# Kernel tuning notes

Measured on AMD Instinct MI355X. Metric: run time of the kernel, lower is better.

## Reference

```python
import jax, jax.numpy as jnp
import numpy as np

DEPTH, DIM, DH, H, DQ, V = 4, 1024, 4096, 8, 128, 32000
B, L = 2, 1024


def setup_inputs() -> dict:
    key = jax.random.key(0)
    ks = iter(jax.random.split(key, 48))
    def nrm(shape, scale=1.0):
        return jax.random.normal(next(ks), shape, jnp.float32) * scale
    d = {}
    d["x"] = nrm((B, L, V))
    d["tin_w"] = nrm((DIM, V), V ** -0.5)
    d["tin_b"] = nrm((DIM,), 0.02)
    d["tout_w"] = nrm((V, DIM), DIM ** -0.5)
    d["tout_b"] = nrm((V,), 0.02)
    d["wq_w"] = nrm((DEPTH, H * DQ, DIM), DIM ** -0.5)
    d["wq_b"] = nrm((DEPTH, H * DQ), 0.02)
    d["wk_w"] = nrm((DEPTH, H * DQ, DIM), DIM ** -0.5)
    d["wk_b"] = nrm((DEPTH, H * DQ), 0.02)
    d["wv_w"] = nrm((DEPTH, H * DQ, DIM), DIM ** -0.5)
    d["wv_b"] = nrm((DEPTH, H * DQ), 0.02)
    d["wo_w"] = nrm((DEPTH, DIM, H * DQ), (H * DQ) ** -0.5)
    d["wo_b"] = nrm((DEPTH, DIM), 0.02)
    d["f1_w"] = nrm((DEPTH, DH, DIM), DIM ** -0.5)
    d["f1_b"] = nrm((DEPTH, DH), 0.02)
    d["f2_w"] = nrm((DEPTH, DIM, DH), DH ** -0.5)
    d["f2_b"] = nrm((DEPTH, DIM), 0.02)
    d["phz_re"] = nrm((DEPTH, H, DQ))
    d["phz_im"] = nrm((DEPTH, H, DQ))
    d["amp"] = nrm((DEPTH, H))
    d["lc_re"] = nrm((DEPTH, H, DQ, DQ), 0.02)
    d["lc_im"] = nrm((DEPTH, H, DQ, DQ), 0.02)
    return d


def _layernorm(x):
    m = x.mean(-1, keepdims=True)
    v = ((x - m) ** 2).mean(-1, keepdims=True)
    return (x - m) * jax.lax.rsqrt(v + 1e-5)


def _retention(x, qw, qb, kw, kb, vw, vb, ow, ob, pre, pim, amp, lcr, lci):
    b, l, _ = x.shape
    q = (x @ qw.T + qb).reshape(b, l, H, DQ)
    k = (x @ kw.T + kb).reshape(b, l, H, DQ)
    v = (x @ vw.T + vb).reshape(b, l, H, DQ)
    pz = pre + 1j * pim                              # [H,DQ] complex
    phase = pz / jnp.abs(pz)                         # unit modulus
    a = jax.nn.sigmoid(amp)                          # [H]
    phazor = phase * a[:, None]
    n = jnp.arange(l)
    pp = phase[None, :, :] ** n[:, None, None]       # [L,H,DQ]
    pp_inv = phase[None, :, :] ** (-n)[:, None, None]
    php = phazor[None, :, :] ** n[:, None, None]
    lc = jax.lax.stop_gradient(lcr + 1j * lci)       # [H,DQ,DQ], detached in torch
    qc = q.astype(jnp.complex64)
    kc = k.astype(jnp.complex64)
    vc = v.astype(jnp.complex64)
    cross = jnp.einsum('blhd,lhd,hde->blhe', qc, php * phazor[None], lc)
    tril = n[:, None] >= n[None, :]
    expn = jnp.where(tril, n[:, None] - n[None, :], 0)           # [L,L]
    mask = jnp.where(tril[None], a[:, None, None] ** expn[None], 0.0)  # [H,L,L]
    qk = jnp.einsum('blhd,bmhd->bhlm', qc * pp[None], kc * pp_inv[None])
    inner = jnp.einsum('bhlm,bmhd->blhd', qk * mask[None].astype(jnp.complex64), vc)
    y = jax.nn.silu((inner + cross).real).reshape(b, l, H * DQ)
    return y @ ow.T + ob


def reference(x, tin_w, tin_b, tout_w, tout_b, wq_w, wq_b, wk_w, wk_b, wv_w, wv_b,
              wo_w, wo_b, f1_w, f1_b, f2_w, f2_b, phz_re, phz_im, amp, lc_re, lc_im):
    h = x @ tin_w.T + tin_b
    for i in range(DEPTH):
        r = _retention(_layernorm(h), wq_w[i], wq_b[i], wk_w[i], wk_b[i],
                       wv_w[i], wv_b[i], wo_w[i], wo_b[i],
                       phz_re[i], phz_im[i], amp[i], lc_re[i], lc_im[i])
        h = h + r
        f = _layernorm(h)
        f = jax.nn.silu(f @ f1_w[i].T + f1_b[i]) @ f2_w[i].T + f2_b[i]
        h = h + f
    return h @ tout_w.T + tout_b
```

## Files before the change

kernel.cpp:

```cpp
#include <hip/hip_runtime.h>
#include <hip/hip_bf16.h>
#include <stdint.h>

#define DEPTH 4
#define DIM   1024
#define DH    4096
#define NH    8
#define DQ    128
#define VOC   32000
#define BATCH 2
#define SEQ   1024
#define ROWS  (BATCH*SEQ)

#define PQKV  ((long long)ROWS*DIM)
#define PQKV3 ((long long)ROWS*3*DIM)
#define PROT  ((long long)BATCH*NH*SEQ*2*DQ)
#define PVT   ((long long)BATCH*NH*DQ*SEQ)
#define PS    ((long long)BATCH*NH*SEQ*SEQ)
#define PMID  ((long long)ROWS*DH)
#define PY    ((long long)ROWS*DIM)

typedef __hip_bfloat16 bf16;
using f32x4  = __attribute__((ext_vector_type(4))) float;
using bf16x8 = __attribute__((ext_vector_type(8))) __bf16;

__device__ __forceinline__ unsigned short bcu(bf16 h) {
  return __builtin_bit_cast(unsigned short, h);
}

__device__ __forceinline__ void wpair(bf16* p, long long off, long long plane, float v) {
  bf16 hi = __float2bfloat16(v);
  p[off] = hi;
  p[off + plane] = __float2bfloat16(v - __bfloat162float(hi));
}

__device__ __forceinline__ void gload_lds16(const void* g, void* l) {
  __builtin_amdgcn_global_load_lds(
      (const __attribute__((address_space(1))) void*)g,
      (__attribute__((address_space(3))) void*)(uintptr_t)l,
      16, 0, 0);
}

#define BM 128
#define BN 128
#define BKK 64
#define PL 16384

template<int EPI, int SA, int SB>
__global__ __launch_bounds__(256, (SA || SB) ? 2 : 4)
void gemm_bt(const bf16* __restrict__ A, long long sA, long long pA, int lda,
             const bf16* __restrict__ B, long long sB, long long pB, int ldb, int bmod,
             void* __restrict__ Cv, long long sC, long long pC, int ldc,
             const float* __restrict__ bias, int hmod,
             int M, int N, int K, int ksplit, int causal)
{
  __shared__ int4 sbuf[1024 * (2 + SA + SB)];
  char* Asb = (char*)sbuf;
  char* Bsb = Asb + PL * (1 + SA);

  const int tid  = threadIdx.x;
  const int lane = tid & 63;
  const int wave = tid >> 6;
  const int wr   = wave >> 1;
  const int wc   = wave & 1;
  const int z    = blockIdx.z;
  const int zb   = z / ksplit;
  const int ks   = z - zb * ksplit;
  const int Kc   = K / ksplit;
  const int k0   = ks * Kc;
  const int tm   = blockIdx.x * BM;
  const int tn   = blockIdx.y * BN;

  if (causal == 1 && tn >= tm + BM) return;
  int kend = k0 + Kc;
  if (causal == 2) {
    kend = min(kend, tm + BM);
    if (kend <= k0) return;
  }

  const bf16* Ab = A + (long long)zb * sA;
  const bf16* Bb = B + (long long)(zb % bmod) * sB;

  f32x4 acc[4][4] = {};

  for (int kt = k0; kt < kend; kt += BKK) {
#pragma unroll
    for (int j = 0; j < 4; ++j) {
      int slot0 = j*256 + wave*64;
      int i = slot0 + lane;
      int row = i >> 3;
      int gc  = (i & 7) ^ (row & 7);
      long long ga = (long long)(tm + row) * lda + kt + gc*8;
      long long gb = (long long)(tn + row) * ldb + kt + gc*8;
      gload_lds16(Ab + ga, Asb + slot0*16);
      if (SA) gload_lds16(Ab + pA + ga, Asb + PL + slot0*16);
      gload_lds16(Bb + gb, Bsb + slot0*16);
      if (SB) gload_lds16(Bb + pB + gb, Bsb + PL + slot0*16);
    }
    __syncthreads();
#pragma unroll
    for (int kh = 0; kh < 2; ++kh) {
      const int cb = kh*4 + (lane >> 4);
      int4 avh[4], bvh[4], avl[4], bvl[4];
#pragma unroll
      for (int mi = 0; mi < 4; ++mi) {
        int m = wr*64 + mi*16 + (lane & 15);
        int off = m*128 + ((cb ^ (m & 7)) << 4);
        avh[mi] = *(const int4*)(Asb + off);
        if (SA) avl[mi] = *(const int4*)(Asb + PL + off);
      }
#pragma unroll
      for (int nj = 0; nj < 4; ++nj) {
        int n = wc*64 + nj*16 + (lane & 15);
        int off = n*128 + ((cb ^ (n & 7)) << 4);
        bvh[nj] = *(const int4*)(Bsb + off);
        if (SB) bvl[nj] = *(const int4*)(Bsb + PL + off);
      }
#pragma unroll
      for (int mi = 0; mi < 4; ++mi)
#pragma unroll
        for (int nj = 0; nj < 4; ++nj)
          acc[mi][nj] = __builtin_amdgcn_mfma_f32_16x16x32_bf16(
              __builtin_bit_cast(bf16x8, avh[mi]),
              __builtin_bit_cast(bf16x8, bvh[nj]), acc[mi][nj], 0, 0, 0);
      if (SA)
#pragma unroll
        for (int mi = 0; mi < 4; ++mi)
#pragma unroll
          for (int nj = 0; nj < 4; ++nj)
            acc[mi][nj] = __builtin_amdgcn_mfma_f32_16x16x32_bf16(
                __builtin_bit_cast(bf16x8, avl[mi]),
                __builtin_bit_cast(bf16x8, bvh[nj]), acc[mi][nj], 0, 0, 0);
      if (SB)
#pragma unroll
        for (int mi = 0; mi < 4; ++mi)
#pragma unroll
          for (int nj = 0; nj < 4; ++nj)
            acc[mi][nj] = __builtin_amdgcn_mfma_f32_16x16x32_bf16(
                __builtin_bit_cast(bf16x8, avh[mi]),
                __builtin_bit_cast(bf16x8, bvl[nj]), acc[mi][nj], 0, 0, 0);
    }
    __syncthreads();
  }

  const float* dtab = (EPI == 7) ? bias + (zb % hmod) * (SEQ + 1) : nullptr;
  const int col = lane & 15;
  const int rb  = (lane >> 4) << 2;
  float* Cf = (float*)Cv + (long long)zb * sC;
  bf16*  Ch = (bf16*) Cv + (long long)zb * sC;

#pragma unroll
  for (int mi = 0; mi < 4; ++mi)
#pragma unroll
    for (int nj = 0; nj < 4; ++nj) {
      long long gn = tn + wc*64 + nj*16 + col;
      float bv_ = (EPI != 7 && bias && ks == 0) ? bias[gn] : 0.f;
#pragma unroll
      for (int r = 0; r < 4; ++r) {
        long long gm = tm + wr*64 + mi*16 + rb + r;
        float v = acc[mi][nj][r] + bv_;
        long long off = gm * (long long)ldc + gn;
        if (EPI == 0)      Cf[off] = v;
        else if (EPI == 3) { if (ksplit > 1) atomicAdd(&Cf[off], v); else Cf[off] += v; }
        else if (EPI == 5) wpair(Ch, off, pC, v);
        else if (EPI == 6) wpair(Ch, off, pC, v / (1.f + __expf(-v)));
        else {
          long long dlt = gm - gn;
          float dcy = (dlt >= 0) ? dtab[dlt] : 0.f;
          Ch[off] = __float2bfloat16(acc[mi][nj][r] * dcy);
        }
      }
    }
}

__global__ void castw_kernel(const float* __restrict__ wq, const float* __restrict__ wk,
                             const float* __restrict__ wv, const float* __restrict__ wo,
                             const float* __restrict__ f1, const float* __restrict__ f2,
                             bf16* __restrict__ Wqkv, bf16* __restrict__ Wol,
                             bf16* __restrict__ Wf1, bf16* __restrict__ Wf2) {
  const long long S1 = (long long)DIM*DIM;
  const long long S4 = S1 >> 2;
  const long long WP = 3*S1;
  long long i = (long long)blockIdx.x * blockDim.x + threadIdx.x;
  const float* src; bf16 *hi, *lo; long long j4;
  if (i < 3*S4) {
    int t = (int)(i / S4);
    src = (t == 0) ? wq : (t == 1) ? wk : wv;
    j4 = i - (long long)t * S4;
    hi = Wqkv + (long long)t * S1; lo = hi + WP;
  } else if (i < 4*S4)  { src = wo; j4 = i - 3*S4; hi = Wol; lo = Wol + S1; }
  else if (i < 8*S4)    { src = f1; j4 = i - 4*S4; hi = Wf1; lo = Wf1 + 4*S1; }
  else if (i < 12*S4)   { src = f2; j4 = i - 8*S4; hi = Wf2; lo = nullptr; }
  else return;
  float4 v = ((const float4*)src)[j4];
  bf16 h0 = __float2bfloat16(v.x), h1 = __float2bfloat16(v.y);
  bf16 h2 = __float2bfloat16(v.z), h3 = __float2bfloat16(v.w);
  ((ushort4*)hi)[j4] = ushort4{bcu(h0), bcu(h1), bcu(h2), bcu(h3)};
  if (lo) {
    bf16 l0 = __float2bfloat16(v.x - __bfloat162float(h0));
    bf16 l1 = __float2bfloat16(v.y - __bfloat162float(h1));
    bf16 l2 = __float2bfloat16(v.z - __bfloat162float(h2));
    bf16 l3 = __float2bfloat16(v.w - __bfloat162float(h3));
    ((ushort4*)lo)[j4] = ushort4{bcu(l0), bcu(l1), bcu(l2), bcu(l3)};
  }
}

#define MISC_LC   (NH*DQ*DQ)
#define MISC_B3   (MISC_LC + 3*DIM)
#define MISC_DC   (MISC_B3 + NH*(SEQ+1))
#define MISC_ZR   (MISC_DC + (BATCH*NH*SEQ*DQ)/4)
__global__ void misc_kernel(const float* __restrict__ lcr, const float* __restrict__ lci,
                            bf16* __restrict__ lc,
                            const float* __restrict__ bq, const float* __restrict__ bk,
                            const float* __restrict__ bv, float* __restrict__ qkvbi,
                            const float* __restrict__ amp, float* __restrict__ dtab,
                            float4* __restrict__ retz) {
  long long i = (long long)blockIdx.x * blockDim.x + threadIdx.x;
  if (i < MISC_LC) {
    int d = i & 127, e = (i >> 7) & 127, h = i >> 14;
    float vr = lcr[((long long)h*DQ + d)*DQ + e];
    float vi = lci[((long long)h*DQ + d)*DQ + e];
    long long dst = ((long long)h*DQ + e)*(2*DQ) + d;
    lc[dst]      = __float2bfloat16(vr);
    lc[dst + DQ] = __float2bfloat16(-vi);
  } else if (i < MISC_B3) {
    int j = (int)(i - MISC_LC);
    qkvbi[j] = (j < DIM) ? bq[j] : (j < 2*DIM) ? bk[j - DIM] : bv[j - 2*DIM];
  } else if (i < MISC_DC) {
    int j = (int)(i - MISC_B3);
    int h = j / (SEQ+1), n = j % (SEQ+1);
    float a = 1.f / (1.f + __expf(-amp[h]));
    dtab[j] = powf(a, (float)n);
  } else if (i < MISC_ZR) {
    retz[i - MISC_DC] = float4{0.f, 0.f, 0.f, 0.f};
  }
}

#define TIN_X4 ((long long)ROWS*VOC/4)
#define TIN_W4 (TIN_X4 + (long long)DIM*VOC/4)
#define TIN_H4 (TIN_W4 + (long long)ROWS*DIM/4)
__global__ void tinprep_kernel(const float* __restrict__ x, bf16* __restrict__ xb,
                               const float* __restrict__ tw, bf16* __restrict__ twb,
                               float4* __restrict__ hz) {
  long long i = (long long)blockIdx.x * blockDim.x + threadIdx.x;
  const float* src; bf16* dst; long long j;
  if (i < TIN_X4)      { src = x;  dst = xb;  j = i; }
  else if (i < TIN_W4) { src = tw; dst = twb; j = i - TIN_X4; }
  else if (i < TIN_H4) { hz[i - TIN_W4] = float4{0.f,0.f,0.f,0.f}; return; }
  else return;
  float4 v = ((const float4*)src)[j];
  ushort4 o{bcu(__float2bfloat16(v.x)), bcu(__float2bfloat16(v.y)),
            bcu(__float2bfloat16(v.z)), bcu(__float2bfloat16(v.w))};
  ((ushort4*)dst)[j] = o;
}

#define TAIL_H (PQKV)
#define TAIL_W (TAIL_H + (long long)VOC*DIM/4)
__global__ void tailprep_kernel(const float* __restrict__ h, bf16* __restrict__ hb,
                                const float* __restrict__ tw, bf16* __restrict__ twb) {
  long long i = (long long)blockIdx.x * blockDim.x + threadIdx.x;
  if (i < TAIL_H) {
    float v = h[i];
    bf16 hi = __float2bfloat16(v);
    hb[i] = hi;
    hb[i + PQKV] = __float2bfloat16(v - __bfloat162float(hi));
  } else if (i < TAIL_W) {
    long long j = i - TAIL_H;
    float4 v = ((const float4*)tw)[j];
    ushort4 o{bcu(__float2bfloat16(v.x)), bcu(__float2bfloat16(v.y)),
              bcu(__float2bfloat16(v.z)), bcu(__float2bfloat16(v.w))};
    ((ushort4*)twb)[j] = o;
  }
}

__global__ void ln_kernel(const float* __restrict__ in, bf16* __restrict__ out) {
  const int row = blockIdx.x;
  const int tid = threadIdx.x;
  const float4 v = ((const float4*)(in + (size_t)row*DIM))[tid];
  float s  = v.x + v.y + v.z + v.w;
  float s2 = v.x*v.x + v.y*v.y + v.z*v.z + v.w*v.w;
#pragma unroll
  for (int o = 32; o > 0; o >>= 1) { s += __shfl_xor(s, o); s2 += __shfl_xor(s2, o); }
  __shared__ float red[8];
  const int wv = tid >> 6;
  if ((tid & 63) == 0) { red[wv] = s; red[4 + wv] = s2; }
  __syncthreads();
  s  = red[0] + red[1] + red[2] + red[3];
  s2 = red[4] + red[5] + red[6] + red[7];
  const float mean = s * (1.f / DIM);
  const float var  = s2 * (1.f / DIM) - mean * mean;
  const float inv  = rsqrtf(var + 1e-5f);
  long long base = (long long)row*DIM + tid*4;
  wpair(out, base + 0, PQKV, (v.x - mean) * inv);
  wpair(out, base + 1, PQKV, (v.y - mean) * inv);
  wpair(out, base + 2, PQKV, (v.z - mean) * inv);
  wpair(out, base + 3, PQKV, (v.w - mean) * inv);
}

__global__ void rotate_kernel(const bf16* __restrict__ qkv,
                              const float* __restrict__ pre, const float* __restrict__ pim,
                              const float* __restrict__ dtab,
                              bf16* __restrict__ qrot, bf16* __restrict__ krot,
                              bf16* __restrict__ qwb) {
  const int d = threadIdx.x, l = blockIdx.x, h = blockIdx.y, b = blockIdx.z;
  const float tr = pre[h*DQ + d], ti = pim[h*DQ + d];
  const float theta = atan2f(ti, tr);
  const long long rowb = (long long)(b*SEQ + l)*(3*DIM) + h*DQ + d;
  const float qv = __bfloat162float(qkv[rowb]) + __bfloat162float(qkv[rowb + PQKV3]);
  const float kv = __bfloat162float(qkv[rowb + DIM]) + __bfloat162float(qkv[rowb + DIM + PQKV3]);
  float sn, cs;
  sincosf(theta * (float)l, &sn, &cs);
  const long long dst = ((long long)(b*NH + h)*SEQ + l)*(2*DQ) + d;
  qrot[dst]      = __float2bfloat16(qv * cs);
  qrot[dst + DQ] = __float2bfloat16(qv * sn);
  krot[dst]      = __float2bfloat16(kv * cs);
  krot[dst + DQ] = __float2bfloat16(kv * sn);
  float sn2, cs2;
  sincosf(theta * (float)(l + 1), &sn2, &cs2);
  const float ad = dtab[h*(SEQ+1) + l + 1];
  qwb[dst]      = __float2bfloat16(qv * ad * cs2);
  qwb[dst + DQ] = __float2bfloat16(qv * ad * sn2);
}

__global__ void vt_kernel(const bf16* __restrict__ qkv, bf16* __restrict__ vt) {
  __shared__ float tile[64][65];
  const int t  = threadIdx.x;
  const int c  = t & 63, r4 = t >> 6;
  const int m0 = blockIdx.x * 64;
  const int d0 = blockIdx.y * 64;
  const int h  = blockIdx.z & (NH - 1);
  const int b  = blockIdx.z >> 3;
#pragma unroll
  for (int rr = 0; rr < 64; rr += 4) {
    const int m = m0 + rr + r4;
    const long long src = (long long)(b*SEQ + m)*(3*DIM) + 2*DIM + h*DQ + d0 + c;
    tile[rr + r4][c] = __bfloat162float(qkv[src]) + __bfloat162float(qkv[src + PQKV3]);
  }
  __syncthreads();
#pragma unroll
  for (int rr = 0; rr < 64; rr += 4) {
    const int d = rr + r4;
    vt[((long long)(b*NH + h)*DQ + d0 + d)*SEQ + m0 + c] = __float2bfloat16(tile[c][d]);
  }
}

__global__ void siluret_kernel(const float* __restrict__ ret, bf16* __restrict__ y) {
  const int d = threadIdx.x, l = blockIdx.x, h = blockIdx.y, b = blockIdx.z;
  float r = ret[((long long)(b*NH + h)*SEQ + l)*DQ + d];
  float s = r / (1.f + __expf(-r));
  wpair(y, ((long long)(b*SEQ + l)*NH + h)*DQ + d, PY, s);
}

extern "C" void kernel_launch(void* const* d_in, const int* in_sizes, int n_in,
                              void* d_out, int out_size, void* d_ws, size_t ws_size,
                              hipStream_t stream) {
  const float* x      = (const float*)d_in[0];
  const float* tin_w  = (const float*)d_in[1];
  const float* tin_b  = (const float*)d_in[2];
  const float* tout_w = (const float*)d_in[3];
  const float* tout_b = (const float*)d_in[4];
  const float* wq_w   = (const float*)d_in[5];
  const float* wq_b   = (const float*)d_in[6];
  const float* wk_w   = (const float*)d_in[7];
  const float* wk_b   = (const float*)d_in[8];
  const float* wv_w   = (const float*)d_in[9];
  const float* wv_b   = (const float*)d_in[10];
  const float* wo_w   = (const float*)d_in[11];
  const float* wo_b   = (const float*)d_in[12];
  const float* f1_w   = (const float*)d_in[13];
  const float* f1_b   = (const float*)d_in[14];
  const float* f2_w   = (const float*)d_in[15];
  const float* f2_b   = (const float*)d_in[16];
  const float* phz_re = (const float*)d_in[17];
  const float* phz_im = (const float*)d_in[18];
  const float* amp    = (const float*)d_in[19];
  const float* lc_re  = (const float*)d_in[20];
  const float* lc_im  = (const float*)d_in[21];
  (void)in_sizes; (void)n_in; (void)out_size; (void)ws_size;

  char* w = (char*)d_ws;
  auto alloc = [&](size_t bytes) {
    char* p = w; w += (bytes + 255) & ~(size_t)255; return p;
  };
  auto palloc = [&](long long elems) {
    return (bf16*)alloc((size_t)elems * 2 * 2);
  };

  const long long WP = 3LL*DIM*DIM;
  float* h     = (float*)alloc((size_t)ROWS*DIM*4);
  float* ret   = (float*)alloc((size_t)BATCH*NH*SEQ*DQ*4);
  float* qkvbi = (float*)alloc((size_t)3*DIM*4);
  float* dtab  = (float*)alloc((size_t)NH*(SEQ+1)*4);
  bf16*  hb    = palloc(PQKV);
  bf16*  Wqkv  = palloc(WP);
  bf16*  Wol   = palloc((long long)DIM*DIM);
  bf16*  Wf1l  = palloc((long long)DH*DIM);
  bf16*  Wf2l  = (bf16*)alloc((size_t)DIM*DH*2);
  bf16*  qkvb  = palloc(PQKV3);
  bf16*  lcc   = (bf16*)alloc((size_t)NH*DQ*2*DQ*2);
  bf16*  Wbig  = (bf16*)alloc((size_t)DIM*VOC*2);
  bf16*  qrot  = (bf16*)alloc((size_t)PROT*2);
  bf16*  krot  = (bf16*)alloc((size_t)PROT*2);
  bf16*  qwb   = (bf16*)alloc((size_t)PROT*2);
  bf16*  vtb   = (bf16*)alloc((size_t)PVT*2);
  bf16*  Sb    = (bf16*)alloc((size_t)PS*2);
  bf16*  mid   = palloc(PMID);
  bf16*  xb = (bf16*)d_out;
  bf16*  yb = qkvb;

  auto gemm = [&](int epi, int sa, int sb, const bf16* A, long long sA, long long pA, int lda,
                  const bf16* B, long long sB, long long pB, int ldb, int bmod,
                  void* C, long long sC, long long pC, int ldc,
                  const float* bias, int hmod, int M, int N, int K, int batch,
                  int ksplit, int causal) {
    dim3 g(M / BM, N / BN, batch * ksplit), blk(256);
    if (epi == 3 && !sa && !sb)      gemm_bt<3,0,0><<<g, blk, 0, stream>>>(A,sA,pA,lda,B,sB,pB,ldb,bmod,C,sC,pC,ldc,bias,hmod,M,N,K,ksplit,causal);
    else if (epi == 7)               gemm_bt<7,0,0><<<g, blk, 0, stream>>>(A,sA,pA,lda,B,sB,pB,ldb,bmod,C,sC,pC,ldc,bias,hmod,M,N,K,ksplit,causal);
    else if (epi == 0 && sa && !sb)  gemm_bt<0,1,0><<<g, blk, 0, stream>>>(A,sA,pA,lda,B,sB,pB,ldb,bmod,C,sC,pC,ldc,bias,hmod,M,N,K,ksplit,causal);
    else if (epi == 3 && sa && !sb)  gemm_bt<3,1,0><<<g, blk, 0, stream>>>(A,sA,pA,lda,B,sB,pB,ldb,bmod,C,sC,pC,ldc,bias,hmod,M,N,K,ksplit,causal);
    else if (epi == 3)               gemm_bt<3,1,1><<<g, blk, 0, stream>>>(A,sA,pA,lda,B,sB,pB,ldb,bmod,C,sC,pC,ldc,bias,hmod,M,N,K,ksplit,causal);
    else if (epi == 5)               gemm_bt<5,1,1><<<g, blk, 0, stream>>>(A,sA,pA,lda,B,sB,pB,ldb,bmod,C,sC,pC,ldc,bias,hmod,M,N,K,ksplit,causal);
    else if (epi == 6)               gemm_bt<6,1,1><<<g, blk, 0, stream>>>(A,sA,pA,lda,B,sB,pB,ldb,bmod,C,sC,pC,ldc,bias,hmod,M,N,K,ksplit,causal);
  };
  const int BIG = 1 << 30;

  tinprep_kernel<<<dim3((unsigned)((TIN_H4 + 255) / 256)), dim3(256), 0, stream>>>(
      x, xb, tin_w, Wbig, (float4*)h);
  gemm(3, 0, 0, xb, 0, 0, VOC, Wbig, 0, 0, VOC, BIG, h, 0, 0, DIM, tin_b, 1,
       ROWS, DIM, VOC, 1, 10, 0);

  for (int i = 0; i < DEPTH; ++i) {
    {
      long long tot4 = 12LL * ((long long)DIM*DIM >> 2);
      castw_kernel<<<dim3((unsigned)((tot4 + 255) / 256)), dim3(256), 0, stream>>>(
          wq_w + (size_t)i*DIM*DIM, wk_w + (size_t)i*DIM*DIM, wv_w + (size_t)i*DIM*DIM,
          wo_w + (size_t)i*DIM*DIM, f1_w + (size_t)i*DH*DIM, f2_w + (size_t)i*DIM*DH,
          Wqkv, Wol, Wf1l, Wf2l);
      misc_kernel<<<dim3((unsigned)((MISC_ZR + 255) / 256)), dim3(256), 0, stream>>>(
          lc_re + (size_t)i*NH*DQ*DQ, lc_im + (size_t)i*NH*DQ*DQ, lcc,
          wq_b + i*DIM, wk_b + i*DIM, wv_b + i*DIM, qkvbi,
          amp + i*NH, dtab, (float4*)ret);
    }

    ln_kernel<<<ROWS, 256, 0, stream>>>(h, hb);
    gemm(5, 1, 1, hb, 0, PQKV, DIM, Wqkv, 0, WP, DIM, BIG,
         qkvb, 0, PQKV3, 3*DIM, qkvbi, 1, ROWS, 3*DIM, DIM, 1, 1, 0);
    rotate_kernel<<<dim3(SEQ, NH, BATCH), DQ, 0, stream>>>(
        qkvb, phz_re + i*NH*DQ, phz_im + i*NH*DQ, dtab, qrot, krot, qwb);
    vt_kernel<<<dim3(SEQ/64, DQ/64, BATCH*NH), 256, 0, stream>>>(qkvb, vtb);
    gemm(7, 0, 0, qrot, (long long)SEQ*2*DQ, 0, 2*DQ,
         krot, (long long)SEQ*2*DQ, 0, 2*DQ, BIG,
         Sb, (long long)SEQ*SEQ, 0, SEQ, dtab, NH, SEQ, SEQ, 2*DQ, BATCH*NH, 1, 1);
    gemm(3, 0, 0, Sb, (long long)SEQ*SEQ, 0, SEQ,
         vtb, (long long)DQ*SEQ, 0, SEQ, BIG,
         ret, (long long)SEQ*DQ, 0, DQ, nullptr, 1, SEQ, DQ, SEQ, BATCH*NH, 4, 2);
    gemm(3, 0, 0, qwb, (long long)SEQ*2*DQ, 0, 2*DQ,
         lcc, (long long)DQ*2*DQ, 0, 2*DQ, NH,
         ret, (long long)SEQ*DQ, 0, DQ, nullptr, 1, SEQ, DQ, 2*DQ, BATCH*NH, 2, 0);
    siluret_kernel<<<dim3(SEQ, NH, BATCH), DQ, 0, stream>>>(ret, yb);
    gemm(3, 1, 1, yb, 0, PY, DIM, Wol, 0, (long long)DIM*DIM, DIM, BIG,
         h, 0, 0, DIM, wo_b + i*DIM, 1, ROWS, DIM, DIM, 1, 2, 0);

    ln_kernel<<<ROWS, 256, 0, stream>>>(h, hb);
    gemm(6, 1, 1, hb, 0, PQKV, DIM, Wf1l, 0, (long long)DH*DIM, DIM, BIG,
         mid, 0, PMID, DH, f1_b + i*DH, 1, ROWS, DH, DIM, 1, 1, 0);
    gemm(3, 1, 0, mid, 0, PMID, DH, Wf2l, 0, 0, DH, BIG,
         h, 0, 0, DIM, f2_b + i*DIM, 1, ROWS, DIM, DH, 1, 4, 0);
  }

  tailprep_kernel<<<dim3((unsigned)((TAIL_W + 255) / 256)), dim3(256), 0, stream>>>(
      h, hb, tout_w, Wbig);
  gemm(0, 1, 0, hb, 0, PQKV, DIM, Wbig, 0, 0, DIM, BIG,
       (float*)d_out, 0, 0, VOC, tout_b, 1, ROWS, VOC, DIM, 1, 1, 0);
}
```

Measured before the change: 1.814 ms.

## Fuse cross-term GEMM into retention S·V GEMM via concatenated K dimension

The cross term (qw @ lc) is folded into the S·V GEMM by widening its K dimension: the qw block is stored in the first 256 columns of an extended score buffer and lc in the first 256 columns of an extended V-transpose buffer, so one GEMM computes both. This removes one GEMM launch and one atomic-accumulate pass over the output. The weight-cast and misc prep kernels are merged into a single launch, atan2 for the phases is precomputed once per layer, and the layernorm stores are vectorized. The causal K bound is shifted to include the prefix columns, at the cost of larger buffers and a more complex indexing scheme.

Result: faster. 1.739 ms, median of 2 (-4.1%).

```diff
diff --git a/kernel.cpp b/kernel.cpp
--- a/kernel.cpp
+++ b/kernel.cpp
@@ -11,12 +11,12 @@
 #define BATCH 2
 #define SEQ   1024
 #define ROWS  (BATCH*SEQ)
+#define CROSSK 256
+#define LDS_X (CROSSK + SEQ)
 
 #define PQKV  ((long long)ROWS*DIM)
 #define PQKV3 ((long long)ROWS*3*DIM)
 #define PROT  ((long long)BATCH*NH*SEQ*2*DQ)
-#define PVT   ((long long)BATCH*NH*DQ*SEQ)
-#define PS    ((long long)BATCH*NH*SEQ*SEQ)
 #define PMID  ((long long)ROWS*DH)
 #define PY    ((long long)ROWS*DIM)
 
@@ -74,7 +74,7 @@
   if (causal == 1 && tn >= tm + BM) return;
   int kend = k0 + Kc;
   if (causal == 2) {
-    kend = min(kend, tm + BM);
+    kend = min(kend, tm + BM + CROSSK);
     if (kend <= k0) return;
   }
 
@@ -173,66 +173,77 @@
     }
 }
 
-__global__ void castw_kernel(const float* __restrict__ wq, const float* __restrict__ wk,
-                             const float* __restrict__ wv, const float* __restrict__ wo,
-                             const float* __restrict__ f1, const float* __restrict__ f2,
-                             bf16* __restrict__ Wqkv, bf16* __restrict__ Wol,
-                             bf16* __restrict__ Wf1, bf16* __restrict__ Wf2) {
-  const long long S1 = (long long)DIM*DIM;
-  const long long S4 = S1 >> 2;
-  const long long WP = 3*S1;
-  long long i = (long long)blockIdx.x * blockDim.x + threadIdx.x;
-  const float* src; bf16 *hi, *lo; long long j4;
-  if (i < 3*S4) {
-    int t = (int)(i / S4);
-    src = (t == 0) ? wq : (t == 1) ? wk : wv;
-    j4 = i - (long long)t * S4;
-    hi = Wqkv + (long long)t * S1; lo = hi + WP;
-  } else if (i < 4*S4)  { src = wo; j4 = i - 3*S4; hi = Wol; lo = Wol + S1; }
-  else if (i < 8*S4)    { src = f1; j4 = i - 4*S4; hi = Wf1; lo = Wf1 + 4*S1; }
-  else if (i < 12*S4)   { src = f2; j4 = i - 8*S4; hi = Wf2; lo = nullptr; }
-  else return;
-  float4 v = ((const float4*)src)[j4];
-  bf16 h0 = __float2bfloat16(v.x), h1 = __float2bfloat16(v.y);
-  bf16 h2 = __float2bfloat16(v.z), h3 = __float2bfloat16(v.w);
-  ((ushort4*)hi)[j4] = ushort4{bcu(h0), bcu(h1), bcu(h2), bcu(h3)};
-  if (lo) {
-    bf16 l0 = __float2bfloat16(v.x - __bfloat162float(h0));
-    bf16 l1 = __float2bfloat16(v.y - __bfloat162float(h1));
-    bf16 l2 = __float2bfloat16(v.z - __bfloat162float(h2));
-    bf16 l3 = __float2bfloat16(v.w - __bfloat162float(h3));
-    ((ushort4*)lo)[j4] = ushort4{bcu(l0), bcu(l1), bcu(l2), bcu(l3)};
-  }
-}
-
-#define MISC_LC   (NH*DQ*DQ)
-#define MISC_B3   (MISC_LC + 3*DIM)
-#define MISC_DC   (MISC_B3 + NH*(SEQ+1))
-#define MISC_ZR   (MISC_DC + (BATCH*NH*SEQ*DQ)/4)
-__global__ void misc_kernel(const float* __restrict__ lcr, const float* __restrict__ lci,
-                            bf16* __restrict__ lc,
+#define MC_LC (NH*DQ*DQ)
+#define MC_TH (MC_LC + NH*DQ)
+#define MC_B3 (MC_TH + 3*DIM)
+#define MC_DC (MC_B3 + NH*(SEQ+1))
+#define MC_ZR (MC_DC + (BATCH*NH*SEQ*DQ)/4)
+__global__ void prep_kernel(const float* __restrict__ wq, const float* __restrict__ wk,
+                            const float* __restrict__ wv, const float* __restrict__ wo,
+                            const float* __restrict__ f1, const float* __restrict__ f2,
+                            bf16* __restrict__ Wqkv, bf16* __restrict__ Wol,
+                            bf16* __restrict__ Wf1, bf16* __restrict__ Wf2,
+                            const float* __restrict__ lcr, const float* __restrict__ lci,
+                            bf16* __restrict__ vte,
+                            const float* __restrict__ pre, const float* __restrict__ pim,
+                            float* __restrict__ theta,
                             const float* __restrict__ bq, const float* __restrict__ bk,
                             const float* __restrict__ bv, float* __restrict__ qkvbi,
                             const float* __restrict__ amp, float* __restrict__ dtab,
                             float4* __restrict__ retz) {
+  const long long S1 = (long long)DIM*DIM;
+  const long long S4 = S1 >> 2;
+  const long long WPq = 3*S1;
+  const long long CW4 = 12*S4;
   long long i = (long long)blockIdx.x * blockDim.x + threadIdx.x;
-  if (i < MISC_LC) {
-    int d = i & 127, e = (i >> 7) & 127, h = i >> 14;
+  if (i < CW4) {
+    const float* src; bf16 *hi, *lo; long long j4;
+    if (i < 3*S4) {
+      int t = (int)(i / S4);
+      src = (t == 0) ? wq : (t == 1) ? wk : wv;
+      j4 = i - (long long)t * S4;
+      hi = Wqkv + (long long)t * S1; lo = hi + WPq;
+    } else if (i < 4*S4)  { src = wo; j4 = i - 3*S4; hi = Wol; lo = Wol + S1; }
+    else if (i < 8*S4)    { src = f1; j4 = i - 4*S4; hi = Wf1; lo = Wf1 + 4*S1; }
+    else                  { src = f2; j4 = i - 8*S4; hi = Wf2; lo = nullptr; }
+    float4 v = ((const float4*)src)[j4];
+    bf16 h0 = __float2bfloat16(v.x), h1 = __float2bfloat16(v.y);
+    bf16 h2 = __float2bfloat16(v.z), h3 = __float2bfloat16(v.w);
+    ((ushort4*)hi)[j4] = ushort4{bcu(h0), bcu(h1), bcu(h2), bcu(h3)};
+    if (lo) {
+      bf16 l0 = __float2bfloat16(v.x - __bfloat162float(h0));
+      bf16 l1 = __float2bfloat16(v.y - __bfloat162float(h1));
+      bf16 l2 = __float2bfloat16(v.z - __bfloat162float(h2));
+      bf16 l3 = __float2bfloat16(v.w - __bfloat162float(h3));
+      ((ushort4*)lo)[j4] = ushort4{bcu(l0), bcu(l1), bcu(l2), bcu(l3)};
+    }
+    return;
+  }
+  long long j = i - CW4;
+  if (j < MC_LC) {
+    int d = (int)(j & 127), e = (int)((j >> 7) & 127), h = (int)(j >> 14);
     float vr = lcr[((long long)h*DQ + d)*DQ + e];
     float vi = lci[((long long)h*DQ + d)*DQ + e];
-    long long dst = ((long long)h*DQ + e)*(2*DQ) + d;
-    lc[dst]      = __float2bfloat16(vr);
-    lc[dst + DQ] = __float2bfloat16(-vi);
-  } else if (i < MISC_B3) {
-    int j = (int)(i - MISC_LC);
-    qkvbi[j] = (j < DIM) ? bq[j] : (j < 2*DIM) ? bk[j - DIM] : bv[j - 2*DIM];
-  } else if (i < MISC_DC) {
-    int j = (int)(i - MISC_B3);
-    int h = j / (SEQ+1), n = j % (SEQ+1);
+    bf16 br = __float2bfloat16(vr), bi = __float2bfloat16(-vi);
+#pragma unroll
+    for (int b = 0; b < BATCH; ++b) {
+      long long base = ((long long)(b*NH + h)*DQ + e) * LDS_X;
+      vte[base + d]      = br;
+      vte[base + DQ + d] = bi;
+    }
+  } else if (j < MC_TH) {
+    int t = (int)(j - MC_LC);
+    theta[t] = atan2f(pim[t], pre[t]);
+  } else if (j < MC_B3) {
+    int t = (int)(j - MC_TH);
+    qkvbi[t] = (t < DIM) ? bq[t] : (t < 2*DIM) ? bk[t - DIM] : bv[t - 2*DIM];
+  } else if (j < MC_DC) {
+    int t = (int)(j - MC_B3);
+    int h = t / (SEQ+1), n = t % (SEQ+1);
     float a = 1.f / (1.f + __expf(-amp[h]));
-    dtab[j] = powf(a, (float)n);
-  } else if (i < MISC_ZR) {
-    retz[i - MISC_DC] = float4{0.f, 0.f, 0.f, 0.f};
+    dtab[t] = powf(a, (float)n);
+  } else if (j < MC_ZR) {
+    retz[j - MC_DC] = float4{0.f, 0.f, 0.f, 0.f};
   }
 }
 
@@ -290,21 +301,25 @@
   const float mean = s * (1.f / DIM);
   const float var  = s2 * (1.f / DIM) - mean * mean;
   const float inv  = rsqrtf(var + 1e-5f);
-  long long base = (long long)row*DIM + tid*4;
-  wpair(out, base + 0, PQKV, (v.x - mean) * inv);
-  wpair(out, base + 1, PQKV, (v.y - mean) * inv);
-  wpair(out, base + 2, PQKV, (v.z - mean) * inv);
-  wpair(out, base + 3, PQKV, (v.w - mean) * inv);
+  float e0 = (v.x - mean) * inv, e1 = (v.y - mean) * inv;
+  float e2 = (v.z - mean) * inv, e3 = (v.w - mean) * inv;
+  bf16 h0 = __float2bfloat16(e0), h1 = __float2bfloat16(e1);
+  bf16 h2 = __float2bfloat16(e2), h3 = __float2bfloat16(e3);
+  bf16 l0 = __float2bfloat16(e0 - __bfloat162float(h0));
+  bf16 l1 = __float2bfloat16(e1 - __bfloat162float(h1));
+  bf16 l2 = __float2bfloat16(e2 - __bfloat162float(h2));
+  bf16 l3 = __float2bfloat16(e3 - __bfloat162float(h3));
+  ((ushort4*)(out + (size_t)row*DIM))[tid]        = ushort4{bcu(h0), bcu(h1), bcu(h2), bcu(h3)};
+  ((ushort4*)(out + PQKV + (size_t)row*DIM))[tid] = ushort4{bcu(l0), bcu(l1), bcu(l2), bcu(l3)};
 }
 
 __global__ void rotate_kernel(const bf16* __restrict__ qkv,
-                              const float* __restrict__ pre, const float* __restrict__ pim,
+                              const float* __restrict__ theta_t,
                               const float* __restrict__ dtab,
                               bf16* __restrict__ qrot, bf16* __restrict__ krot,
-                              bf16* __restrict__ qwb) {
+                              bf16* __restrict__ SbX) {
   const int d = threadIdx.x, l = blockIdx.x, h = blockIdx.y, b = blockIdx.z;
-  const float tr = pre[h*DQ + d], ti = pim[h*DQ + d];
-  const float theta = atan2f(ti, tr);
+  const float theta = theta_t[h*DQ + d];
   const long long rowb = (long long)(b*SEQ + l)*(3*DIM) + h*DQ + d;
   const float qv = __bfloat162float(qkv[rowb]) + __bfloat162float(qkv[rowb + PQKV3]);
   const float kv = __bfloat162float(qkv[rowb + DIM]) + __bfloat162float(qkv[rowb + DIM + PQKV3]);
@@ -318,11 +333,12 @@
   float sn2, cs2;
   sincosf(theta * (float)(l + 1), &sn2, &cs2);
   const float ad = dtab[h*(SEQ+1) + l + 1];
-  qwb[dst]      = __float2bfloat16(qv * ad * cs2);
-  qwb[dst + DQ] = __float2bfloat16(qv * ad * sn2);
-}
-
-__global__ void vt_kernel(const bf16* __restrict__ qkv, bf16* __restrict__ vt) {
+  const long long qw = ((long long)(b*NH + h)*SEQ + l)*LDS_X + d;
+  SbX[qw]      = __float2bfloat16(qv * ad * cs2);
+  SbX[qw + DQ] = __float2bfloat16(qv * ad * sn2);
+}
+
+__global__ void vt_kernel(const bf16* __restrict__ qkv, bf16* __restrict__ vte) {
   __shared__ float tile[64][65];
   const int t  = threadIdx.x;
   const int c  = t & 63, r4 = t >> 6;
@@ -340,7 +356,8 @@
 #pragma unroll
   for (int rr = 0; rr < 64; rr += 4) {
     const int d = rr + r4;
-    vt[((long long)(b*NH + h)*DQ + d0 + d)*SEQ + m0 + c] = __float2bfloat16(tile[c][d]);
+    vte[((long long)(b*NH + h)*DQ + d0 + d)*LDS_X + CROSSK + m0 + c] =
+        __float2bfloat16(tile[c][d]);
   }
 }
 
@@ -391,19 +408,18 @@
   float* ret   = (float*)alloc((size_t)BATCH*NH*SEQ*DQ*4);
   float* qkvbi = (float*)alloc((size_t)3*DIM*4);
   float* dtab  = (float*)alloc((size_t)NH*(SEQ+1)*4);
+  float* theta = (float*)alloc((size_t)NH*DQ*4);
   bf16*  hb    = palloc(PQKV);
   bf16*  Wqkv  = palloc(WP);
   bf16*  Wol   = palloc((long long)DIM*DIM);
   bf16*  Wf1l  = palloc((long long)DH*DIM);
   bf16*  Wf2l  = (bf16*)alloc((size_t)DIM*DH*2);
   bf16*  qkvb  = palloc(PQKV3);
-  bf16*  lcc   = (bf16*)alloc((size_t)NH*DQ*2*DQ*2);
   bf16*  Wbig  = (bf16*)alloc((size_t)DIM*VOC*2);
   bf16*  qrot  = (bf16*)alloc((size_t)PROT*2);
   bf16*  krot  = (bf16*)alloc((size_t)PROT*2);
-  bf16*  qwb   = (bf16*)alloc((size_t)PROT*2);
-  bf16*  vtb   = (bf16*)alloc((size_t)PVT*2);
-  bf16*  Sb    = (bf16*)alloc((size_t)PS*2);
+  bf16*  SbX   = (bf16*)alloc((size_t)BATCH*NH*SEQ*LDS_X*2);
+  bf16*  vte   = (bf16*)alloc((size_t)BATCH*NH*DQ*LDS_X*2);
   bf16*  mid   = palloc(PMID);
   bf16*  xb = (bf16*)d_out;
   bf16*  yb = qkvb;
@@ -431,13 +447,13 @@
 
   for (int i = 0; i < DEPTH; ++i) {
     {
-      long long tot4 = 12LL * ((long long)DIM*DIM >> 2);
-      castw_kernel<<<dim3((unsigned)((tot4 + 255) / 256)), dim3(256), 0, stream>>>(
+      long long tot = 12LL*((long long)DIM*DIM >> 2) + MC_ZR;
+      prep_kernel<<<dim3((unsigned)((tot + 255) / 256)), dim3(256), 0, stream>>>(
           wq_w + (size_t)i*DIM*DIM, wk_w + (size_t)i*DIM*DIM, wv_w + (size_t)i*DIM*DIM,
           wo_w + (size_t)i*DIM*DIM, f1_w + (size_t)i*DH*DIM, f2_w + (size_t)i*DIM*DH,
-          Wqkv, Wol, Wf1l, Wf2l);
-      misc_kernel<<<dim3((unsigned)((MISC_ZR + 255) / 256)), dim3(256), 0, stream>>>(
-          lc_re + (size_t)i*NH*DQ*DQ, lc_im + (size_t)i*NH*DQ*DQ, lcc,
+          Wqkv, Wol, Wf1l, Wf2l,
+          lc_re + (size_t)i*NH*DQ*DQ, lc_im + (size_t)i*NH*DQ*DQ, vte,
+          phz_re + i*NH*DQ, phz_im + i*NH*DQ, theta,
           wq_b + i*DIM, wk_b + i*DIM, wv_b + i*DIM, qkvbi,
           amp + i*NH, dtab, (float4*)ret);
     }
@@ -446,17 +462,15 @@
     gemm(5, 1, 1, hb, 0, PQKV, DIM, Wqkv, 0, WP, DIM, BIG,
          qkvb, 0, PQKV3, 3*DIM, qkvbi, 1, ROWS, 3*DIM, DIM, 1, 1, 0);
     rotate_kernel<<<dim3(SEQ, NH, BATCH), DQ, 0, stream>>>(
-        qkvb, phz_re + i*NH*DQ, phz_im + i*NH*DQ, dtab, qrot, krot, qwb);
-    vt_kernel<<<dim3(SEQ/64, DQ/64, BATCH*NH), 256, 0, stream>>>(qkvb, vtb);
+        qkvb, theta, dtab, qrot, krot, SbX);
+    vt_kernel<<<dim3(SEQ/64, DQ/64, BATCH*NH), 256, 0, stream>>>(qkvb, vte);
     gemm(7, 0, 0, qrot, (long long)SEQ*2*DQ, 0, 2*DQ,
          krot, (long long)SEQ*2*DQ, 0, 2*DQ, BIG,
-         Sb, (long long)SEQ*SEQ, 0, SEQ, dtab, NH, SEQ, SEQ, 2*DQ, BATCH*NH, 1, 1);
-    gemm(3, 0, 0, Sb, (long long)SEQ*SEQ, 0, SEQ,
-         vtb, (long long)DQ*SEQ, 0, SEQ, BIG,
-         ret, (long long)SEQ*DQ, 0, DQ, nullptr, 1, SEQ, DQ, SEQ, BATCH*NH, 4, 2);
-    gemm(3, 0, 0, qwb, (long long)SEQ*2*DQ, 0, 2*DQ,
-         lcc, (long long)DQ*2*DQ, 0, 2*DQ, NH,
-         ret, (long long)SEQ*DQ, 0, DQ, nullptr, 1, SEQ, DQ, 2*DQ, BATCH*NH, 2, 0);
+         SbX + CROSSK, (long long)SEQ*LDS_X, 0, LDS_X, dtab, NH,
+         SEQ, SEQ, 2*DQ, BATCH*NH, 1, 1);
+    gemm(3, 0, 0, SbX, (long long)SEQ*LDS_X, 0, LDS_X,
+         vte, (long long)DQ*LDS_X, 0, LDS_X, BIG,
+         ret, (long long)SEQ*DQ, 0, DQ, nullptr, 1, SEQ, DQ, LDS_X, BATCH*NH, 4, 2);
     siluret_kernel<<<dim3(SEQ, NH, BATCH), DQ, 0, stream>>>(ret, yb);
     gemm(3, 1, 1, yb, 0, PY, DIM, Wol, 0, (long long)DIM*DIM, DIM, BIG,
          h, 0, 0, DIM, wo_b + i*DIM, 1, ROWS, DIM, DIM, 1, 2, 0);
```
